# Kernel tuning notes

Measured on AMD Instinct MI355X. Metric: run time of the kernel, lower is better.

Reference implementation:

```python
import jax, jax.numpy as jnp
import numpy as np

B, S, H = 2, 2048, 2048
NH, KVH, HD = 16, 4, 128
THETA = 10000.0


def setup_inputs() -> dict:
    key = jax.random.key(0)
    k1, k2, k3, k4, k5 = jax.random.split(key, 5)
    scale = 1.0 / np.sqrt(H)
    return {
        "hidden_states": jax.random.normal(k1, (B, S, H), dtype=jnp.float32),
        "Wq": jax.random.normal(k2, (H, NH * HD), dtype=jnp.float32) * scale,
        "Wk": jax.random.normal(k3, (H, KVH * HD), dtype=jnp.float32) * scale,
        "Wv": jax.random.normal(k4, (H, KVH * HD), dtype=jnp.float32) * scale,
        "Wo": jax.random.normal(k5, (NH * HD, H), dtype=jnp.float32) * scale,
    }


def _rotate_half(x):
    x1, x2 = x[..., : HD // 2], x[..., HD // 2 :]
    return jnp.concatenate((-x2, x1), axis=-1)


def _rope_cos_sin(seq_len):
    # inv_freq: [HD/2]
    inv_freq = 1.0 / (THETA ** (jnp.arange(0, HD, 2, dtype=jnp.float32) / HD))
    pos = jnp.arange(seq_len, dtype=jnp.float32)
    freqs = pos[:, None] * inv_freq[None, :]          # [S, HD/2]
    emb = jnp.concatenate((freqs, freqs), axis=-1)    # [S, HD]
    return jnp.cos(emb), jnp.sin(emb)


def reference(hidden_states, Wq, Wk, Wv, Wo):
    b, s, _ = hidden_states.shape
    n_rep = NH // KVH

    # projections -> [B, S, heads, HD]
    q = (hidden_states @ Wq).reshape(b, s, NH, HD)
    k = (hidden_states @ Wk).reshape(b, s, KVH, HD)
    v = (hidden_states @ Wv).reshape(b, s, KVH, HD)

    # RoPE (cos/sin broadcast over head dim, matching cos.unsqueeze(-2))
    cos, sin = _rope_cos_sin(s)
    cos = cos[None, :, None, :]  # [1, S, 1, HD]
    sin = sin[None, :, None, :]
    q = q * cos + _rotate_half(q) * sin
    k = k * cos + _rotate_half(k) * sin

    # repeat_kv: [B, S, KVH, HD] -> [B, S, NH, HD]
    k = jnp.repeat(k, n_rep, axis=2)
    v = jnp.repeat(v, n_rep, axis=2)

    # causal SDPA
    scores = jnp.einsum("bqhd,bkhd->bhqk", q, k) / jnp.sqrt(jnp.float32(HD))
    causal = jnp.tril(jnp.ones((s, s), dtype=bool))
    scores = jnp.where(causal[None, None], scores, jnp.finfo(scores.dtype).min)
    probs = jax.nn.softmax(scores, axis=-1)
    ctx = jnp.einsum("bhqk,bkhd->bqhd", probs, v)     # [B, S, NH, HD]

    out = ctx.reshape(b, s, NH * HD) @ Wo             # [B, S, H]
    return out
```

## Files before the change

kernel.cpp:

```cpp
#include <hip/hip_runtime.h>
#include <stdint.h>
#include <math.h>

#define BB 2
#define SS 2048
#define HH 2048
#define NH 16
#define KVH 4
#define HD 128
#define BSZ (BB*SS)
#define QW (NH*HD)
#define KVW (KVH*HD)

typedef __attribute__((ext_vector_type(8))) short s16x8;
typedef __attribute__((ext_vector_type(4))) float f32x4;

typedef const unsigned int __attribute__((address_space(1)))* gas_ptr;
typedef unsigned int __attribute__((address_space(3)))* las_ptr;

__device__ __forceinline__ unsigned short f2b(float x) {
    unsigned u = __builtin_bit_cast(unsigned, x);
    unsigned r = u + 0x7fffu + ((u >> 16) & 1u);
    return (unsigned short)(r >> 16);
}
__device__ __forceinline__ float b2f(unsigned short h) {
    unsigned u = ((unsigned)h) << 16;
    return __builtin_bit_cast(float, u);
}

__device__ __forceinline__ void gload_lds16(const void* g, void* l) {
    __builtin_amdgcn_global_load_lds((gas_ptr)g, (las_ptr)l, 16, 0, 0);
}

template<int FN>
__device__ __forceinline__ void stage_half(
    const unsigned short* __restrict__ src, int rowbase, int k0,
    unsigned short* dst)
{
    const int tid = threadIdx.x;
#pragma unroll
    for (int q = 0; q < 2; ++q) {
        int row = (tid >> 3) + q * 64;
        int sl  = (tid & 7) ^ (row & 7);
        gload_lds16(src + (size_t)(rowbase + row) * HH + k0 + sl * 8,
                    dst + (q * 512 + tid) * 8);
    }
}

__device__ __forceinline__ s16x8 ldsr(const unsigned short* base,
                                      int r, int kh, int quad)
{
    return *(const s16x8*)(base + r * 64 + (((kh * 4 + quad) ^ (r & 7)) * 8));
}

#define SBAR() do { __builtin_amdgcn_sched_barrier(0); \
                    __builtin_amdgcn_s_barrier();       \
                    __builtin_amdgcn_sched_barrier(0); } while (0)

template<int FN>
__device__ __forceinline__ void gemm8p(
    const unsigned short* __restrict__ A,
    const unsigned short* __restrict__ Bt,
    int m0, int c0, unsigned short* lds, f32x4 acc[8][FN])
{
    constexpr int NT    = HH / 64;
    constexpr int BUFE  = (2 + FN / 2) * 8192;
    constexpr int ABOFF = (FN / 2) * 8192;
    const int tid  = threadIdx.x;
    const int lane = tid & 63, wave = tid >> 6;
    const int quad = lane >> 4, l15 = lane & 15;
    const int wm = wave >> 2, wn = wave & 3;
    const int arow0 = wm * 128 + l15;
    const int brow0 = wn * (FN * 16) + l15;

#pragma unroll
    for (int i = 0; i < 8; ++i)
#pragma unroll
        for (int fc = 0; fc < FN; ++fc) acc[i][fc] = (f32x4){0.f, 0.f, 0.f, 0.f};

    unsigned short* buf0 = lds;
    unsigned short* buf1 = lds + BUFE;

    stage_half<FN>(Bt, c0, 0, buf0);
    if constexpr (FN == 4) stage_half<FN>(Bt, c0 + 128, 0, buf0 + 8192);
    stage_half<FN>(A, m0, 0, buf0 + ABOFF);
    stage_half<FN>(A, m0 + 128, 0, buf0 + ABOFF + 8192);
    stage_half<FN>(Bt, c0, 64, buf1);
    if constexpr (FN == 4) {
        stage_half<FN>(Bt, c0 + 128, 64, buf1 + 8192);
        asm volatile("s_waitcnt vmcnt(4)" ::: "memory");
    } else {
        asm volatile("s_waitcnt vmcnt(2)" ::: "memory");
    }
    SBAR();

#pragma unroll 2
    for (int T = 0; T < NT; ++T) {
        unsigned short* buf = (T & 1) ? buf1 : buf0;
        unsigned short* nbuf = (T & 1) ? buf0 : buf1;
        const unsigned short* Bb = buf;
        const unsigned short* Ab = buf + ABOFF;
        const int k1 = (T + 1) * 64, k2 = (T + 2) * 64;

        s16x8 b[FN][2], a01[2][2];
#pragma unroll
        for (int fc = 0; fc < FN; ++fc)
#pragma unroll
            for (int kh = 0; kh < 2; ++kh)
                b[fc][kh] = ldsr(Bb, brow0 + fc * 16, kh, quad);
#pragma unroll
        for (int fr = 0; fr < 2; ++fr)
#pragma unroll
            for (int kh = 0; kh < 2; ++kh)
                a01[fr][kh] = ldsr(Ab, arow0 + fr * 16, kh, quad);
        if (T + 1 < NT) stage_half<FN>(A, m0, k1, nbuf + ABOFF);
        SBAR();
        __builtin_amdgcn_s_setprio(1);
#pragma unroll
        for (int fr = 0; fr < 2; ++fr)
#pragma unroll
            for (int fc = 0; fc < FN; ++fc)
#pragma unroll
                for (int kh = 0; kh < 2; ++kh)
                    acc[fr][fc] = __builtin_amdgcn_mfma_f32_16x16x32_bf16(
                        a01[fr][kh], b[fc][kh], acc[fr][fc], 0, 0, 0);
        __builtin_amdgcn_s_setprio(0);
        SBAR();

        s16x8 a23[2][2], a45[2][2];
#pragma unroll
        for (int fr = 0; fr < 2; ++fr)
#pragma unroll
            for (int kh = 0; kh < 2; ++kh) {
                a23[fr][kh] = ldsr(Ab, arow0 + (2 + fr) * 16, kh, quad);
                a45[fr][kh] = ldsr(Ab, arow0 + (4 + fr) * 16, kh, quad);
            }
        if (T + 1 < NT) stage_half<FN>(A, m0 + 128, k1, nbuf + ABOFF + 8192);
        SBAR();
        __builtin_amdgcn_s_setprio(1);
#pragma unroll
        for (int fr = 0; fr < 2; ++fr)
#pragma unroll
            for (int fc = 0; fc < FN; ++fc)
#pragma unroll
                for (int kh = 0; kh < 2; ++kh)
                    acc[2 + fr][fc] = __builtin_amdgcn_mfma_f32_16x16x32_bf16(
                        a23[fr][kh], b[fc][kh], acc[2 + fr][fc], 0, 0, 0);
        __builtin_amdgcn_s_setprio(0);
        SBAR();

        s16x8 a67[2][2];
#pragma unroll
        for (int fr = 0; fr < 2; ++fr)
#pragma unroll
            for (int kh = 0; kh < 2; ++kh)
                a67[fr][kh] = ldsr(Ab, arow0 + (6 + fr) * 16, kh, quad);
        if (T + 2 < NT) stage_half<FN>(Bt, c0, k2, buf);
        SBAR();
        __builtin_amdgcn_s_setprio(1);
#pragma unroll
        for (int fr = 0; fr < 2; ++fr)
#pragma unroll
            for (int fc = 0; fc < FN; ++fc)
#pragma unroll
                for (int kh = 0; kh < 2; ++kh)
                    acc[4 + fr][fc] = __builtin_amdgcn_mfma_f32_16x16x32_bf16(
                        a45[fr][kh], b[fc][kh], acc[4 + fr][fc], 0, 0, 0);
        __builtin_amdgcn_s_setprio(0);
        SBAR();

        if constexpr (FN == 4) {
            if (T + 2 < NT) stage_half<FN>(Bt, c0 + 128, k2, buf + 8192);
        }
        __builtin_amdgcn_sched_barrier(0);
        if (T <= NT - 3) {
            if constexpr (FN == 4) asm volatile("s_waitcnt vmcnt(4)" ::: "memory");
            else                   asm volatile("s_waitcnt vmcnt(2)" ::: "memory");
        } else if (T == NT - 2) {
            asm volatile("s_waitcnt vmcnt(0)" ::: "memory");
        }
        SBAR();
        __builtin_amdgcn_s_setprio(1);
#pragma unroll
        for (int fr = 0; fr < 2; ++fr)
#pragma unroll
            for (int fc = 0; fc < FN; ++fc)
#pragma unroll
                for (int kh = 0; kh < 2; ++kh)
                    acc[6 + fr][fc] = __builtin_amdgcn_mfma_f32_16x16x32_bf16(
                        a67[fr][kh], b[fc][kh], acc[6 + fr][fc], 0, 0, 0);
        __builtin_amdgcn_s_setprio(0);
        SBAR();
    }
}

__global__ __launch_bounds__(512, 2) void gemm_qkv(
    const unsigned short* __restrict__ Ah,
    const unsigned short* __restrict__ Wqt,
    const unsigned short* __restrict__ Wkt,
    const unsigned short* __restrict__ Wvt,
    unsigned short* __restrict__ Qb,
    unsigned short* __restrict__ Kb,
    unsigned short* __restrict__ Vb)
{
    __shared__ __align__(16) unsigned short lds[2 * 4 * 8192];
    const int id  = blockIdx.y * 12 + blockIdx.x;
    const int swz = (id & 7) * 24 + (id >> 3);
    const int nblk = (swz % 12) * 256;
    const int m0   = (swz / 12) * 256;
    const unsigned short* Bt;
    unsigned short* C;
    int c0, ldc;
    if (nblk < QW)            { Bt = Wqt; C = Qb; c0 = nblk;            ldc = QW;  }
    else if (nblk < QW + KVW) { Bt = Wkt; C = Kb; c0 = nblk - QW;       ldc = KVW; }
    else                      { Bt = Wvt; C = Vb; c0 = nblk - QW - KVW; ldc = KVW; }

    f32x4 acc[8][4];
    gemm8p<4>(Ah, Bt, m0, c0, lds, acc);

    const int tid = threadIdx.x;
    const int lane = tid & 63;
    const int quad = lane >> 4, l15 = lane & 15;
    const int wm = (tid >> 6) >> 2, wn = (tid >> 6) & 3;
#pragma unroll
    for (int fr = 0; fr < 8; ++fr)
#pragma unroll
        for (int fc = 0; fc < 4; ++fc)
#pragma unroll
            for (int r = 0; r < 4; ++r) {
                int row = m0 + wm * 128 + fr * 16 + quad * 4 + r;
                int col = c0 + wn * 64 + fc * 16 + l15;
                C[(size_t)row * ldc + col] = f2b(acc[fr][fc][r]);
            }
}

__global__ __launch_bounds__(512, 2) void gemm_out(
    const unsigned short* __restrict__ ctx,
    const unsigned short* __restrict__ Wot,
    float* __restrict__ out)
{
    __shared__ __align__(16) unsigned short lds[2 * 3 * 8192];
    const int id  = blockIdx.y * 16 + blockIdx.x;
    const int swz = (id & 7) * 32 + (id >> 3);
    const int c0 = (swz & 15) * 128;
    const int m0 = (swz >> 4) * 256;

    f32x4 acc[8][2];
    gemm8p<2>(ctx, Wot, m0, c0, lds, acc);

    const int tid = threadIdx.x;
    const int lane = tid & 63;
    const int quad = lane >> 4, l15 = lane & 15;
    const int wm = (tid >> 6) >> 2, wn = (tid >> 6) & 3;
#pragma unroll
    for (int fr = 0; fr < 8; ++fr)
#pragma unroll
        for (int fc = 0; fc < 2; ++fc)
#pragma unroll
            for (int r = 0; r < 4; ++r) {
                int row = m0 + wm * 128 + fr * 16 + quad * 4 + r;
                int col = c0 + wn * 32 + fc * 16 + l15;
                out[(size_t)row * HH + col] = acc[fr][fc][r];
            }
}

__global__ __launch_bounds__(256) void prep(
    const float* __restrict__ hidden, unsigned short* __restrict__ Ah,
    const float* __restrict__ Wq, const float* __restrict__ Wk,
    const float* __restrict__ Wv, const float* __restrict__ Wo,
    unsigned short* __restrict__ Wqt, unsigned short* __restrict__ Wkt,
    unsigned short* __restrict__ Wvt, unsigned short* __restrict__ Wot)
{
    __shared__ float t[32][33];
    const int bx = blockIdx.x;
    if (bx < 8192) {
        int i = (bx * 256 + threadIdx.x) * 4;
        float4 v = *(const float4*)(hidden + i);
        ushort4 o = make_ushort4(f2b(v.x), f2b(v.y), f2b(v.z), f2b(v.w));
        *(ushort4*)(Ah + i) = o;
        return;
    }
    const int b2 = bx - 8192;
    const int z  = b2 >> 12;
    const int xy = b2 & 4095;
    const float* in;
    unsigned short* out;
    int N;
    if (z == 0)      { in = Wq; out = Wqt; N = QW;  }
    else if (z == 1) { in = Wk; out = Wkt; N = KVW; }
    else if (z == 2) { in = Wv; out = Wvt; N = KVW; }
    else             { in = Wo; out = Wot; N = HH;  }
    const int n0 = (xy & 63) * 32;
    if (n0 >= N) return;
    const int k0 = (xy >> 6) * 32;

    const int c = threadIdx.x & 31, r = threadIdx.x >> 5;
#pragma unroll
    for (int j = 0; j < 4; ++j)
        t[r + j * 8][c] = in[(size_t)(k0 + r + j * 8) * N + n0 + c];
    __syncthreads();
#pragma unroll
    for (int j = 0; j < 4; ++j)
        out[(size_t)(n0 + r + j * 8) * HH + k0 + c] = f2b(t[c][r + j * 8]);
}

__global__ __launch_bounds__(256) void vtrans_bf16(const unsigned short* __restrict__ Vb,
                                                   unsigned short* __restrict__ Vtg)
{
    __shared__ unsigned short t[32][33];
    const int s0 = blockIdx.x * 32, c0 = blockIdx.y * 32, b = blockIdx.z;
    const int cc = threadIdx.x & 31, r = threadIdx.x >> 5;
#pragma unroll
    for (int j = 0; j < 4; ++j)
        t[r + j * 8][cc] = Vb[(size_t)(b * SS + s0 + r + j * 8) * KVW + c0 + cc];
    __syncthreads();
#pragma unroll
    for (int j = 0; j < 4; ++j)
        Vtg[(size_t)(b * KVW + c0 + r + j * 8) * SS + s0 + cc] = t[cc][r + j * 8];
}

__global__ __launch_bounds__(256) void rope_all(unsigned short* __restrict__ Qb,
                                                unsigned short* __restrict__ Kb)
{
    int idx = blockIdx.x * 256 + threadIdx.x;
    const int totalQ = BSZ * NH * 8;
    unsigned short* X;
    int nheads; float mul;
    if (idx < totalQ) { X = Qb; nheads = NH; mul = 0.08838834764831845f; }
    else              { X = Kb; nheads = KVH; mul = 1.0f; idx -= totalQ; }
    const int j0 = (idx & 7) * 8;
    const int t  = idx >> 3;
    const int hh = t % nheads;
    const int bs = t / nheads;
    const float s = (float)(bs & (SS - 1));
    size_t base = (size_t)bs * ((size_t)nheads * HD) + (size_t)hh * HD + j0;
    s16x8 v1 = *(const s16x8*)(X + base);
    s16x8 v2 = *(const s16x8*)(X + base + 64);
    s16x8 o1, o2;
#pragma unroll
    for (int e = 0; e < 8; ++e) {
        float inv = exp2f(-0.2076205063f * (float)(j0 + e));
        float ang = s * inv;
        float c = __cosf(ang), sn = __sinf(ang);
        float x1 = b2f((unsigned short)v1[e]);
        float x2 = b2f((unsigned short)v2[e]);
        o1[e] = (short)f2b((x1 * c - x2 * sn) * mul);
        o2[e] = (short)f2b((x2 * c + x1 * sn) * mul);
    }
    *(s16x8*)(X + base)      = o1;
    *(s16x8*)(X + base + 64) = o2;
}

__global__ __launch_bounds__(256) void attn_mfma(
    const unsigned short* __restrict__ Qb,
    const unsigned short* __restrict__ Kb,
    const unsigned short* __restrict__ Vtg,
    unsigned short* __restrict__ ctx)
{
    const int b   = blockIdx.x;
    const int h   = blockIdx.y;
    const int qtp = 31 - blockIdx.z;
    const int kvh = h >> 2;
    const int q0  = qtp * 64;
    const int tid = threadIdx.x;
    const int lane = tid & 63, wave = tid >> 6;
    const int quad = lane >> 4, l15 = lane & 15;
    const int lo8 = l15 & 7, hi8 = l15 >> 3;

    __shared__ __align__(16) unsigned short Ks[64 * 128];
    __shared__ __align__(16) unsigned short Vt[128 * 64];
    __shared__ __align__(16) unsigned short Ps[4][16 * 64];

    const int krb = tid >> 4;
    const int c8k = tid & 15;
    const int dv  = tid >> 3;
    const int c8v = tid & 7;

    const unsigned short* Kbase = Kb  + (size_t)b * SS * KVW + kvh * HD;
    const unsigned short* Vbase = Vtg + (size_t)(b * KVW + kvh * HD) * SS;

    s16x8 qf[4];
    {
        const unsigned short* qrow =
            Qb + (size_t)(b * SS + q0 + wave * 16 + l15) * QW + h * HD;
#pragma unroll
        for (int dc = 0; dc < 4; ++dc)
            qf[dc] = *(const s16x8*)(qrow + dc * 32 + quad * 8);
    }

    f32x4 oacc[8];
#pragma unroll
    for (int i = 0; i < 8; ++i) oacc[i] = (f32x4){0.f, 0.f, 0.f, 0.f};
    f32x4 lacc = (f32x4){0.f, 0.f, 0.f, 0.f};

    const s16x8 vone = {0x3F80, 0x3F80, 0x3F80, 0x3F80,
                        0x3F80, 0x3F80, 0x3F80, 0x3F80};

    s16x8 kpre[4], vpre[4];
#pragma unroll
    for (int u = 0; u < 4; ++u) {
        kpre[u] = *(const s16x8*)(Kbase + (size_t)(u * 16 + krb) * KVW + c8k * 8);
        vpre[u] = *(const s16x8*)(Vbase + (size_t)(u * 32 + dv) * SS + c8v * 8);
    }

    const int nkt = qtp + 1;
    for (int kt = 0; kt < nkt; ++kt) {
        const int k0 = kt * 64;
        __syncthreads();

#pragma unroll
        for (int u = 0; u < 4; ++u) {
            *(s16x8*)(Ks + (u * 16 + krb) * 128 + ((c8k ^ krb) * 8)) = kpre[u];
            *(s16x8*)(Vt + (u * 32 + dv) * 64 + ((c8v ^ (dv & 7)) * 8)) = vpre[u];
        }
        __syncthreads();

        if (kt + 1 < nkt) {
            const int kn = k0 + 64;
#pragma unroll
            for (int u = 0; u < 4; ++u) {
                kpre[u] = *(const s16x8*)(Kbase + (size_t)(kn + u * 16 + krb) * KVW + c8k * 8);
                vpre[u] = *(const s16x8*)(Vbase + (size_t)(u * 32 + dv) * SS + kn + c8v * 8);
            }
        }

        f32x4 sc[4];
#pragma unroll
        for (int tk = 0; tk < 4; ++tk) sc[tk] = (f32x4){0.f, 0.f, 0.f, 0.f};
        __builtin_amdgcn_s_setprio(1);
#pragma unroll
        for (int tk = 0; tk < 4; ++tk) {
#pragma unroll
            for (int dc = 0; dc < 4; ++dc) {
                s16x8 kf = *(const s16x8*)(Ks + (tk * 16 + l15) * 128
                                              + (((dc * 4 + quad) ^ l15) * 8));
                sc[tk] = __builtin_amdgcn_mfma_f32_16x16x32_bf16(qf[dc], kf, sc[tk], 0, 0, 0);
            }
        }
        __builtin_amdgcn_s_setprio(0);

        unsigned short* pw = &Ps[wave][0];
        const bool lastt = (kt == nkt - 1);
#pragma unroll
        for (int tk = 0; tk < 4; ++tk) {
            float p[4];
#pragma unroll
            for (int r = 0; r < 4; ++r)
                p[r] = __expf(sc[tk][r] - 10.0f);
            if (lastt) {
                const int colr = tk * 16 + l15 - wave * 16 - quad * 4;
#pragma unroll
                for (int r = 0; r < 4; ++r)
                    if (colr > r) p[r] = 0.f;
            }
            const int cb = tk * 2 + hi8;
            const int row0 = quad * 4;
#pragma unroll
            for (int r = 0; r < 4; ++r)
                pw[(row0 + r) * 64 + (((cb ^ ((row0 + r) & 7)) << 3) | lo8)] = f2b(p[r]);
        }

        s16x8 pf[2];
#pragma unroll
        for (int kc = 0; kc < 2; ++kc)
            pf[kc] = *(const s16x8*)(pw + l15 * 64 + (((kc * 4 + quad) ^ lo8) << 3));
        __builtin_amdgcn_s_setprio(1);
        lacc = __builtin_amdgcn_mfma_f32_16x16x32_bf16(pf[0], vone, lacc, 0, 0, 0);
        lacc = __builtin_amdgcn_mfma_f32_16x16x32_bf16(pf[1], vone, lacc, 0, 0, 0);
#pragma unroll
        for (int dt = 0; dt < 8; ++dt) {
#pragma unroll
            for (int kc = 0; kc < 2; ++kc) {
                s16x8 vf = *(const s16x8*)(Vt + (dt * 16 + l15) * 64
                                              + (((kc * 4 + quad) ^ lo8) * 8));
                oacc[dt] = __builtin_amdgcn_mfma_f32_16x16x32_bf16(pf[kc], vf, oacc[dt], 0, 0, 0);
            }
        }
        __builtin_amdgcn_s_setprio(0);
    }

    float linv[4];
#pragma unroll
    for (int r = 0; r < 4; ++r) linv[r] = 1.0f / lacc[r];
#pragma unroll
    for (int dt = 0; dt < 8; ++dt)
#pragma unroll
        for (int r = 0; r < 4; ++r) {
            int row = b * SS + q0 + wave * 16 + quad * 4 + r;
            ctx[(size_t)row * QW + h * HD + dt * 16 + l15] =
                f2b(oacc[dt][r] * linv[r]);
        }
}

extern "C" void kernel_launch(void* const* d_in, const int* in_sizes, int n_in,
                              void* d_out, int out_size, void* d_ws, size_t ws_size,
                              hipStream_t stream)
{
    const float* hidden = (const float*)d_in[0];
    const float* Wq = (const float*)d_in[1];
    const float* Wk = (const float*)d_in[2];
    const float* Wv = (const float*)d_in[3];
    const float* Wo = (const float*)d_in[4];
    float* out = (float*)d_out;

    unsigned short* Ah  = (unsigned short*)d_ws;
    unsigned short* Wqt = Ah  + (size_t)BSZ * HH;
    unsigned short* Wkt = Wqt + (size_t)QW * HH;
    unsigned short* Wvt = Wkt + (size_t)KVW * HH;
    unsigned short* Wot = Wvt + (size_t)KVW * HH;
    unsigned short* Qb  = Wot + (size_t)HH * QW;
    unsigned short* Kb  = Qb  + (size_t)BSZ * QW;
    unsigned short* Vb  = Kb  + (size_t)BSZ * KVW;
    unsigned short* ctx = Vb  + (size_t)BSZ * KVW;
    unsigned short* Vtg = ctx + (size_t)BSZ * QW;

    prep<<<24576, 256, 0, stream>>>(hidden, Ah, Wq, Wk, Wv, Wo,
                                    Wqt, Wkt, Wvt, Wot);

    gemm_qkv<<<dim3(12, 16), 512, 0, stream>>>(Ah, Wqt, Wkt, Wvt, Qb, Kb, Vb);

    vtrans_bf16<<<dim3(SS / 32, KVW / 32, BB), 256, 0, stream>>>(Vb, Vtg);

    rope_all<<<(BSZ * (NH + KVH) * 8) / 256, 256, 0, stream>>>(Qb, Kb);

    attn_mfma<<<dim3(BB, NH, SS / 64), 256, 0, stream>>>(Qb, Kb, Vtg, ctx);

    gemm_out<<<dim3(16, 16), 512, 0, stream>>>(ctx, Wot, out);
}
```

Baseline: 273.3 us.

## Pair short and long causal query tiles per block to share K/V loads

Each attention block now handles two query tiles, p and 31-p, so every block does the same total causal work. The K/V tiles staged in shared memory serve both query tiles, which roughly halves K/V global traffic and balances load across a grid that drops from 32 to 16 z-blocks. It also sets launch_bounds(256,2) to hold occupancy despite doubled accumulator registers, at the risk of spills or lower occupancy.

```diff
diff --git a/kernel.cpp b/kernel.cpp
--- a/kernel.cpp
+++ b/kernel.cpp
@@ -351,7 +351,7 @@
     *(s16x8*)(X + base + 64) = o2;
 }
 
-__global__ __launch_bounds__(256) void attn_mfma(
+__global__ __launch_bounds__(256, 2) void attn_mfma(
     const unsigned short* __restrict__ Qb,
     const unsigned short* __restrict__ Kb,
     const unsigned short* __restrict__ Vtg,
@@ -359,9 +359,10 @@
 {
     const int b   = blockIdx.x;
     const int h   = blockIdx.y;
-    const int qtp = 31 - blockIdx.z;
+    const int p   = blockIdx.z;
     const int kvh = h >> 2;
-    const int q0  = qtp * 64;
+    const int q0a = p * 64;
+    const int q0b = (31 - p) * 64;
     const int tid = threadIdx.x;
     const int lane = tid & 63, wave = tid >> 6;
     const int quad = lane >> 4, l15 = lane & 15;
@@ -379,51 +380,33 @@
     const unsigned short* Kbase = Kb  + (size_t)b * SS * KVW + kvh * HD;
     const unsigned short* Vbase = Vtg + (size_t)(b * KVW + kvh * HD) * SS;
 
-    s16x8 qf[4];
+    s16x8 qfa[4], qfb[4];
     {
-        const unsigned short* qrow =
-            Qb + (size_t)(b * SS + q0 + wave * 16 + l15) * QW + h * HD;
-#pragma unroll
-        for (int dc = 0; dc < 4; ++dc)
-            qf[dc] = *(const s16x8*)(qrow + dc * 32 + quad * 8);
-    }
-
-    f32x4 oacc[8];
-#pragma unroll
-    for (int i = 0; i < 8; ++i) oacc[i] = (f32x4){0.f, 0.f, 0.f, 0.f};
-    f32x4 lacc = (f32x4){0.f, 0.f, 0.f, 0.f};
+        const unsigned short* qra =
+            Qb + (size_t)(b * SS + q0a + wave * 16 + l15) * QW + h * HD;
+        const unsigned short* qrb =
+            Qb + (size_t)(b * SS + q0b + wave * 16 + l15) * QW + h * HD;
+#pragma unroll
+        for (int dc = 0; dc < 4; ++dc) {
+            qfa[dc] = *(const s16x8*)(qra + dc * 32 + quad * 8);
+            qfb[dc] = *(const s16x8*)(qrb + dc * 32 + quad * 8);
+        }
+    }
+
+    f32x4 oacca[8], oaccb[8];
+#pragma unroll
+    for (int i = 0; i < 8; ++i) {
+        oacca[i] = (f32x4){0.f, 0.f, 0.f, 0.f};
+        oaccb[i] = (f32x4){0.f, 0.f, 0.f, 0.f};
+    }
+    f32x4 lacca = (f32x4){0.f, 0.f, 0.f, 0.f};
+    f32x4 laccb = (f32x4){0.f, 0.f, 0.f, 0.f};
 
     const s16x8 vone = {0x3F80, 0x3F80, 0x3F80, 0x3F80,
                         0x3F80, 0x3F80, 0x3F80, 0x3F80};
 
-    s16x8 kpre[4], vpre[4];
-#pragma unroll
-    for (int u = 0; u < 4; ++u) {
-        kpre[u] = *(const s16x8*)(Kbase + (size_t)(u * 16 + krb) * KVW + c8k * 8);
-        vpre[u] = *(const s16x8*)(Vbase + (size_t)(u * 32 + dv) * SS + c8v * 8);
-    }
-
-    const int nkt = qtp + 1;
-    for (int kt = 0; kt < nkt; ++kt) {
-        const int k0 = kt * 64;
-        __syncthreads();
-
-#pragma unroll
-        for (int u = 0; u < 4; ++u) {
-            *(s16x8*)(Ks + (u * 16 + krb) * 128 + ((c8k ^ krb) * 8)) = kpre[u];
-            *(s16x8*)(Vt + (u * 32 + dv) * 64 + ((c8v ^ (dv & 7)) * 8)) = vpre[u];
-        }
-        __syncthreads();
-
-        if (kt + 1 < nkt) {
-            const int kn = k0 + 64;
-#pragma unroll
-            for (int u = 0; u < 4; ++u) {
-                kpre[u] = *(const s16x8*)(Kbase + (size_t)(kn + u * 16 + krb) * KVW + c8k * 8);
-                vpre[u] = *(const s16x8*)(Vbase + (size_t)(u * 32 + dv) * SS + kn + c8v * 8);
-            }
-        }
-
+    auto tile_step = [&](const s16x8 (&qf)[4], f32x4 (&oacc)[8],
+                         f32x4& lacc, bool lastt) {
         f32x4 sc[4];
 #pragma unroll
         for (int tk = 0; tk < 4; ++tk) sc[tk] = (f32x4){0.f, 0.f, 0.f, 0.f};
@@ -440,24 +423,23 @@
         __builtin_amdgcn_s_setprio(0);
 
         unsigned short* pw = &Ps[wave][0];
-        const bool lastt = (kt == nkt - 1);
 #pragma unroll
         for (int tk = 0; tk < 4; ++tk) {
-            float p[4];
+            float pv[4];
 #pragma unroll
             for (int r = 0; r < 4; ++r)
-                p[r] = __expf(sc[tk][r] - 10.0f);
+                pv[r] = __expf(sc[tk][r] - 10.0f);
             if (lastt) {
                 const int colr = tk * 16 + l15 - wave * 16 - quad * 4;
 #pragma unroll
                 for (int r = 0; r < 4; ++r)
-                    if (colr > r) p[r] = 0.f;
+                    if (colr > r) pv[r] = 0.f;
             }
             const int cb = tk * 2 + hi8;
             const int row0 = quad * 4;
 #pragma unroll
             for (int r = 0; r < 4; ++r)
-                pw[(row0 + r) * 64 + (((cb ^ ((row0 + r) & 7)) << 3) | lo8)] = f2b(p[r]);
+                pw[(row0 + r) * 64 + (((cb ^ ((row0 + r) & 7)) << 3) | lo8)] = f2b(pv[r]);
         }
 
         s16x8 pf[2];
@@ -477,19 +459,56 @@
             }
         }
         __builtin_amdgcn_s_setprio(0);
-    }
-
-    float linv[4];
-#pragma unroll
-    for (int r = 0; r < 4; ++r) linv[r] = 1.0f / lacc[r];
-#pragma unroll
-    for (int dt = 0; dt < 8; ++dt)
-#pragma unroll
-        for (int r = 0; r < 4; ++r) {
-            int row = b * SS + q0 + wave * 16 + quad * 4 + r;
-            ctx[(size_t)row * QW + h * HD + dt * 16 + l15] =
-                f2b(oacc[dt][r] * linv[r]);
-        }
+    };
+
+    s16x8 kpre[4], vpre[4];
+#pragma unroll
+    for (int u = 0; u < 4; ++u) {
+        kpre[u] = *(const s16x8*)(Kbase + (size_t)(u * 16 + krb) * KVW + c8k * 8);
+        vpre[u] = *(const s16x8*)(Vbase + (size_t)(u * 32 + dv) * SS + c8v * 8);
+    }
+
+    const int nkt = 32 - p;
+    for (int kt = 0; kt < nkt; ++kt) {
+        const int k0 = kt * 64;
+        __syncthreads();
+
+#pragma unroll
+        for (int u = 0; u < 4; ++u) {
+            *(s16x8*)(Ks + (u * 16 + krb) * 128 + ((c8k ^ krb) * 8)) = kpre[u];
+            *(s16x8*)(Vt + (u * 32 + dv) * 64 + ((c8v ^ (dv & 7)) * 8)) = vpre[u];
+        }
+        __syncthreads();
+
+        if (kt + 1 < nkt) {
+            const int kn = k0 + 64;
+#pragma unroll
+            for (int u = 0; u < 4; ++u) {
+                kpre[u] = *(const s16x8*)(Kbase + (size_t)(kn + u * 16 + krb) * KVW + c8k * 8);
+                vpre[u] = *(const s16x8*)(Vbase + (size_t)(u * 32 + dv) * SS + kn + c8v * 8);
+            }
+        }
+
+        tile_step(qfb, oaccb, laccb, kt == nkt - 1);
+        if (kt <= p)
+            tile_step(qfa, oacca, lacca, kt == p);
+    }
+
+    auto write_out = [&](const f32x4 (&oacc)[8], const f32x4& lacc, int q0) {
+        float linv[4];
+#pragma unroll
+        for (int r = 0; r < 4; ++r) linv[r] = 1.0f / lacc[r];
+#pragma unroll
+        for (int dt = 0; dt < 8; ++dt)
+#pragma unroll
+            for (int r = 0; r < 4; ++r) {
+                int row = b * SS + q0 + wave * 16 + quad * 4 + r;
+                ctx[(size_t)row * QW + h * HD + dt * 16 + l15] =
+                    f2b(oacc[dt][r] * linv[r]);
+            }
+    };
+    write_out(oacca, lacca, q0a);
+    write_out(oaccb, laccb, q0b);
 }
 
 extern "C" void kernel_launch(void* const* d_in, const int* in_sizes, int n_in,
@@ -523,7 +542,7 @@
 
     rope_all<<<(BSZ * (NH + KVH) * 8) / 256, 256, 0, stream>>>(Qb, Kb);
 
-    attn_mfma<<<dim3(BB, NH, SS / 64), 256, 0, stream>>>(Qb, Kb, Vtg, ctx);
+    attn_mfma<<<dim3(BB, NH, 16), 256, 0, stream>>>(Qb, Kb, Vtg, ctx);
 
     gemm_out<<<dim3(16, 16), 512, 0, stream>>>(ctx, Wot, out);
 }
```

Measured after the change: 400.8 us. 1.47x slower.
